# Kernel tuning notes

Measured on AMD Instinct MI355X. Metric: run time of the kernel, lower is better.

## Reference

```python
import jax, jax.numpy as jnp
import numpy as np

B, S, D = 2, 4096, 512
H, DK, DV = 8, 64, 64
LN_EPS = 1e-5
ATTN_EPS = 1e-6


def layer_norm(x, g, b):
    mu = jnp.mean(x, axis=-1, keepdims=True)
    var = jnp.var(x, axis=-1, keepdims=True)
    return (x - mu) * jax.lax.rsqrt(var + LN_EPS) * g + b


def setup_inputs() -> dict:
    key = jax.random.key(0)
    ks = jax.random.split(key, 12)
    s = 1.0 / np.sqrt(D)
    inp = {
        "Q": jax.random.normal(ks[0], (B, S, D), jnp.float32),
        "K": jax.random.normal(ks[1], (B, S, D), jnp.float32),
        "V": jax.random.normal(ks[2], (B, S, D), jnp.float32),
        "W_q": jax.random.normal(ks[3], (D, H * DK), jnp.float32) * s,
        "W_k": jax.random.normal(ks[4], (D, H * DK), jnp.float32) * s,
        "W_v": jax.random.normal(ks[5], (D, H * DV), jnp.float32) * s,
        "W_o": jax.random.normal(ks[6], (H * DV, D), jnp.float32) * s,
        "ln1_g": jnp.ones((D,), jnp.float32),
        "ln1_b": jnp.zeros((D,), jnp.float32),
        "ln2_g": jnp.ones((D,), jnp.float32),
        "ln2_b": jnp.zeros((D,), jnp.float32),
        "w1": jax.random.normal(ks[7], (4 * D, D), jnp.float32) * s,  # torch Linear: (out, in)
        "b1": jnp.zeros((4 * D,), jnp.float32),
        "w2": jax.random.normal(ks[8], (D, 4 * D), jnp.float32) * (1.0 / np.sqrt(4 * D)),
        "b2": jnp.zeros((D,), jnp.float32),
    }
    return inp


def reference(Q, K, V, W_q, W_k, W_v, W_o, ln1_g, ln1_b, ln2_g, ln2_b, w1, b1, w2, b2):
    Qn = layer_norm(Q, ln1_g, ln1_b)
    # project and split heads: [B,S,H,dk] -> [B,H,S,dk]
    q = (Qn @ W_q).reshape(B, S, H, DK).transpose(0, 2, 1, 3)
    k = (K @ W_k).reshape(B, S, H, DK).transpose(0, 2, 1, 3)
    v = (V @ W_v).reshape(B, S, H, DV).transpose(0, 2, 1, 3)
    scores = jnp.einsum("bhqd,bhkd->bhqk", q, k) / (np.sqrt(DK) + ATTN_EPS)
    attn = jax.nn.softmax(scores, axis=-1)  # same as max-subtract softmax
    ctx = jnp.einsum("bhqk,bhkd->bhqd", attn, v)
    ctx = ctx.transpose(0, 2, 1, 3).reshape(B, S, H * DV)
    att_out = ctx @ W_o  # dropout = identity (eval)
    X = Q + att_out
    Xn = layer_norm(X, ln2_g, ln2_b)
    h = jax.nn.gelu(Xn @ w1.T + b1, approximate=False)
    ffn = h @ w2.T + b2
    return X + ffn
```

## Files before the change

kernel.cpp:

```cpp
#include <hip/hip_runtime.h>

typedef unsigned short u16;
typedef __attribute__((ext_vector_type(8))) short short8;
typedef __attribute__((ext_vector_type(4))) float f32x4;

struct __align__(8) us4 { u16 x, y, z, w; };
struct __align__(8) ui2 { unsigned x, y; };

#define CEXP (1.44269504089f / (8.0f + 1e-6f))

__device__ __forceinline__ u16 f2bf(float f) {
  unsigned u = __builtin_bit_cast(unsigned, f);
  unsigned r = (u + 0x7FFFu + ((u >> 16) & 1u)) >> 16;
  return (u16)r;
}

__device__ __forceinline__ unsigned pack_bf2_trunc(float a, float b) {
  return __builtin_amdgcn_perm(__builtin_bit_cast(unsigned, b),
                               __builtin_bit_cast(unsigned, a), 0x07060302u);
}

__device__ __forceinline__ void async_load16(const void* g, void* l) {
  __builtin_amdgcn_global_load_lds((const __attribute__((address_space(1))) void*)g,
                                   (__attribute__((address_space(3))) void*)l, 16, 0, 0);
}

__global__ void prep_weights(const float* __restrict__ Wq, const float* __restrict__ Wk,
                             const float* __restrict__ Wv, const float* __restrict__ Wo,
                             const float* __restrict__ w1, const float* __restrict__ w2,
                             u16* __restrict__ wqkvT, u16* __restrict__ woT,
                             u16* __restrict__ w1b, u16* __restrict__ w2b) {
  const int z = blockIdx.y;
  const int stride = gridDim.x * blockDim.x;
  const int i0 = blockIdx.x * blockDim.x + threadIdx.x;
  if (z < 4) {
    const float* src = z == 0 ? Wq : z == 1 ? Wk : z == 2 ? Wv : Wo;
    u16* dst = z < 3 ? wqkvT + z * 512 * 512 : woT;
    const float scale = (z == 0) ? CEXP : 1.0f;
    for (int i = i0; i < 512 * 512; i += stride) {
      int n = i >> 9, k = i & 511;
      dst[i] = f2bf(src[k * 512 + n] * scale);
    }
  } else {
    const float* src = z == 4 ? w1 : w2;
    u16* dst = z == 4 ? w1b : w2b;
    for (int i = i0; i < 2048 * 512; i += stride) dst[i] = f2bf(src[i]);
  }
}

template <bool KV>
__launch_bounds__(128)
__global__ void ln_cast(const float* __restrict__ X, const float* __restrict__ gw,
                        const float* __restrict__ bw, u16* __restrict__ Y,
                        const float* __restrict__ Kin, const float* __restrict__ Vin,
                        u16* __restrict__ Kb, u16* __restrict__ Vb) {
  const int row = blockIdx.x, t = threadIdx.x;
  const size_t base = (size_t)row * 512;
  float4 x = ((const float4*)(X + base))[t];
  float s = x.x + x.y + x.z + x.w;
  float ss = x.x * x.x + x.y * x.y + x.z * x.z + x.w * x.w;
#pragma unroll
  for (int off = 32; off > 0; off >>= 1) {
    s += __shfl_xor(s, off);
    ss += __shfl_xor(ss, off);
  }
  __shared__ float red[4];
  if ((t & 63) == 0) { red[(t >> 6) * 2] = s; red[(t >> 6) * 2 + 1] = ss; }
  __syncthreads();
  const float tot = red[0] + red[2], tss = red[1] + red[3];
  const float mu = tot * (1.0f / 512.0f);
  const float var = tss * (1.0f / 512.0f) - mu * mu;
  const float rs = rsqrtf(var + 1e-5f);
  float4 g4 = ((const float4*)gw)[t];
  float4 b4 = ((const float4*)bw)[t];
  us4 o;
  o.x = f2bf((x.x - mu) * rs * g4.x + b4.x);
  o.y = f2bf((x.y - mu) * rs * g4.y + b4.y);
  o.z = f2bf((x.z - mu) * rs * g4.z + b4.z);
  o.w = f2bf((x.w - mu) * rs * g4.w + b4.w);
  ((us4*)(Y + base))[t] = o;
  if constexpr (KV) {
    float4 k4 = ((const float4*)(Kin + base))[t];
    float4 v4 = ((const float4*)(Vin + base))[t];
    us4 ko, vo;
    ko.x = f2bf(k4.x); ko.y = f2bf(k4.y); ko.z = f2bf(k4.z); ko.w = f2bf(k4.w);
    vo.x = f2bf(v4.x); vo.y = f2bf(v4.y); vo.z = f2bf(v4.z); vo.w = f2bf(v4.w);
    ((us4*)(Kb + base))[t] = ko;
    ((us4*)(Vb + base))[t] = vo;
  }
}

__launch_bounds__(256, 3)
__global__ void gemm_qkv(const u16* __restrict__ Aq, const u16* __restrict__ Ak,
                         const u16* __restrict__ Av, const u16* __restrict__ Bt,
                         u16* __restrict__ qb, u16* __restrict__ kb, u16* __restrict__ vtb) {
  __shared__ __align__(16) u16 sA[128 * 32];
  __shared__ __align__(16) u16 sB[128 * 32];
  const int tid = threadIdx.x;
  const int wave = tid >> 6, lane = tid & 63;
  const int l15 = lane & 15, quad = lane >> 4;
  const int m0 = blockIdx.x * 128, n0 = blockIdx.y * 128;
  const int sel = n0 >> 9;
  const u16* A = sel == 0 ? Aq : sel == 1 ? Ak : Av;
  const int wm = (wave >> 1) * 64, wn = (wave & 1) * 64;
  const int u0 = wave * 64 + lane, u1 = u0 + 256;
  const int K = 512;

  const u16* a0 = A + (size_t)(m0 + (u0 >> 2)) * K + (u0 & 3) * 8;
  const u16* a1 = A + (size_t)(m0 + (u1 >> 2)) * K + (u1 & 3) * 8;
  const u16* b0 = Bt + (size_t)(n0 + (u0 >> 2)) * K + (u0 & 3) * 8;
  const u16* b1p = Bt + (size_t)(n0 + (u1 >> 2)) * K + (u1 & 3) * 8;

  f32x4 acc[4][4] = {};
  for (int k0 = 0; k0 < K; k0 += 32) {
    async_load16(a0 + k0, &sA[wave * 512]);
    async_load16(a1 + k0, &sA[2048 + wave * 512]);
    async_load16(b0 + k0, &sB[wave * 512]);
    async_load16(b1p + k0, &sB[2048 + wave * 512]);
    __syncthreads();
    short8 af[4], bfr[4];
#pragma unroll
    for (int i = 0; i < 4; i++)
      af[i] = *(const short8*)&sA[(wm + i * 16 + l15) * 32 + quad * 8];
#pragma unroll
    for (int j = 0; j < 4; j++)
      bfr[j] = *(const short8*)&sB[(wn + j * 16 + l15) * 32 + quad * 8];
#pragma unroll
    for (int i = 0; i < 4; i++)
#pragma unroll
      for (int j = 0; j < 4; j++)
        acc[i][j] = __builtin_amdgcn_mfma_f32_16x16x32_bf16(af[i], bfr[j], acc[i][j], 0, 0, 0);
    __syncthreads();
  }

#pragma unroll
  for (int i = 0; i < 4; i++) {
#pragma unroll
    for (int j = 0; j < 4; j++) {
      const int ocol = ((n0 + wn) & 511) + j * 16 + l15;
      const int row0 = m0 + wm + i * 16 + quad * 4;
      if (sel < 2) {
        u16* C = sel == 0 ? qb : kb;
#pragma unroll
        for (int r = 0; r < 4; r++) C[(size_t)(row0 + r) * 512 + ocol] = f2bf(acc[i][j][r]);
      } else {
        const int b = row0 >> 12, s0 = row0 & 4095;
        const int hh = ocol >> 6, cc = ocol & 63;
        us4 pk;
        pk.x = f2bf(acc[i][j][0]); pk.y = f2bf(acc[i][j][1]);
        pk.z = f2bf(acc[i][j][2]); pk.w = f2bf(acc[i][j][3]);
        *(us4*)&vtb[((size_t)((b * 8 + hh) * 64 + cc) << 12) + s0] = pk;
      }
    }
  }
}

template <int EP, int TN, int LB>
__launch_bounds__(256, LB)
__global__ void gemm_bt(const u16* __restrict__ A, const u16* __restrict__ Bt,
                        int M, int N, int K, void* __restrict__ Cp,
                        const float* __restrict__ bias, const float* __restrict__ res) {
  constexpr int MI = (TN == 128) ? 4 : 2;
  __shared__ __align__(16) u16 sA[128 * 32];
  __shared__ __align__(16) u16 sB[TN * 32];
  const int tid = threadIdx.x;
  const int wave = tid >> 6, lane = tid & 63;
  const int l15 = lane & 15, quad = lane >> 4;
  const int m0 = blockIdx.x * 128, n0 = blockIdx.y * TN;
  const int wm = (TN == 128) ? (wave >> 1) * 64 : wave * 32;
  const int wn = (TN == 128) ? (wave & 1) * 64 : 0;
  const int u0 = wave * 64 + lane, u1 = u0 + 256;

  const u16* a0 = A + (size_t)(m0 + (u0 >> 2)) * K + (u0 & 3) * 8;
  const u16* a1 = A + (size_t)(m0 + (u1 >> 2)) * K + (u1 & 3) * 8;
  const u16* b0 = Bt + (size_t)(n0 + (u0 >> 2)) * K + (u0 & 3) * 8;

  f32x4 acc[MI][4] = {};
  for (int k0 = 0; k0 < K; k0 += 32) {
    async_load16(a0 + k0, &sA[wave * 512]);
    async_load16(a1 + k0, &sA[2048 + wave * 512]);
    async_load16(b0 + k0, &sB[wave * 512]);
    if constexpr (TN == 128) {
      const u16* b1p = Bt + (size_t)(n0 + (u1 >> 2)) * K + (u1 & 3) * 8;
      async_load16(b1p + k0, &sB[2048 + wave * 512]);
    }
    __syncthreads();
    short8 af[MI], bfr[4];
#pragma unroll
    for (int i = 0; i < MI; i++)
      af[i] = *(const short8*)&sA[(wm + i * 16 + l15) * 32 + quad * 8];
#pragma unroll
    for (int j = 0; j < 4; j++)
      bfr[j] = *(const short8*)&sB[(wn + j * 16 + l15) * 32 + quad * 8];
#pragma unroll
    for (int i = 0; i < MI; i++)
#pragma unroll
      for (int j = 0; j < 4; j++)
        acc[i][j] = __builtin_amdgcn_mfma_f32_16x16x32_bf16(af[i], bfr[j], acc[i][j], 0, 0, 0);
    __syncthreads();
  }

#pragma unroll
  for (int i = 0; i < MI; i++) {
#pragma unroll
    for (int j = 0; j < 4; j++) {
      const int col = n0 + wn + j * 16 + l15;
      const int row0 = m0 + wm + i * 16 + quad * 4;
      if (EP == 2) {
        float* C = (float*)Cp;
#pragma unroll
        for (int r = 0; r < 4; r++) {
          size_t idx = (size_t)(row0 + r) * N + col;
          C[idx] = acc[i][j][r] + res[idx];
        }
      } else if (EP == 3) {
        u16* C = (u16*)Cp;
        const float bv = bias[col];
#pragma unroll
        for (int r = 0; r < 4; r++) {
          float xx = acc[i][j][r] + bv;
          float gl = 0.5f * xx * (1.0f + erff(xx * 0.70710678118f));
          C[(size_t)(row0 + r) * N + col] = f2bf(gl);
        }
      } else {
        float* C = (float*)Cp;
        const float bv = bias[col];
#pragma unroll
        for (int r = 0; r < 4; r++) {
          size_t idx = (size_t)(row0 + r) * N + col;
          C[idx] = acc[i][j][r] + bv + res[idx];
        }
      }
    }
  }
}

__launch_bounds__(256, 3)
__global__ void attn_kernel(const u16* __restrict__ qb, const u16* __restrict__ kb,
                            const u16* __restrict__ vtb, u16* __restrict__ ctx) {
  __shared__ __align__(16) u16 sK[2 * 128 * 32];
  __shared__ __align__(16) u16 sV[4 * 64 * 32];
  __shared__ __align__(16) u16 sP[4 * 32 * 40];
  const int tid = threadIdx.x;
  const int wave = tid >> 6, lane = tid & 63;
  const int l15 = lane & 15, quad = lane >> 4;
  const int bh = blockIdx.y, b = bh >> 3, h = bh & 7;
  const int q0 = blockIdx.x * 128;
  const size_t rb = (size_t)b * 4096;

  short8 qf[2][2];
#pragma unroll
  for (int mi = 0; mi < 2; mi++)
#pragma unroll
    for (int kk = 0; kk < 2; kk++) {
      int row = q0 + wave * 32 + mi * 16 + l15;
      qf[mi][kk] = *(const short8*)&qb[(rb + row) * 512 + h * 64 + kk * 32 + quad * 8];
    }

  f32x4 o_t[2][4] = {};
  float l_part[2] = {0.f, 0.f};
  u16* myP = &sP[wave * 32 * 40];

  for (int j0 = 0; j0 < 4096; j0 += 128) {
#pragma unroll
    for (int r = 0; r < 4; r++) {
      int u = r * 256 + wave * 64 + lane;
      int kk = u >> 9, key = (u >> 2) & 127, c8 = u & 3;
      async_load16(&kb[(rb + j0 + key) * 512 + h * 64 + kk * 32 + c8 * 8],
                   &sK[(r * 256 + wave * 64) * 8]);
    }
#pragma unroll
    for (int r = 0; r < 4; r++) {
      int u = r * 256 + wave * 64 + lane;
      int kk = u >> 8, vc = (u >> 2) & 63, c8 = u & 3;
      async_load16(&vtb[((size_t)(bh * 64 + vc)) * 4096 + j0 + kk * 32 + c8 * 8],
                   &sV[(r * 256 + wave * 64) * 8]);
    }
    __syncthreads();

#pragma unroll
    for (int kk = 0; kk < 4; kk++) {
#pragma unroll
      for (int nh = 0; nh < 2; nh++) {
        const int ni = kk * 2 + nh;
        short8 af0 = *(const short8*)&sK[(ni * 16 + l15) * 32 + quad * 8];
        short8 af1 = *(const short8*)&sK[4096 + (ni * 16 + l15) * 32 + quad * 8];
#pragma unroll
        for (int mi = 0; mi < 2; mi++) {
          f32x4 st = {};
          st = __builtin_amdgcn_mfma_f32_16x16x32_bf16(af0, qf[mi][0], st, 0, 0, 0);
          st = __builtin_amdgcn_mfma_f32_16x16x32_bf16(af1, qf[mi][1], st, 0, 0, 0);
          float p0 = exp2f(st[0]), p1 = exp2f(st[1]);
          float p2 = exp2f(st[2]), p3 = exp2f(st[3]);
          l_part[mi] += (p0 + p1) + (p2 + p3);
          ui2 w;
          w.x = pack_bf2_trunc(p0, p1);
          w.y = pack_bf2_trunc(p2, p3);
          *(ui2*)&myP[(mi * 16 + l15) * 40 + nh * 16 + quad * 4] = w;
        }
      }
      asm volatile("s_waitcnt lgkmcnt(0)" ::: "memory");
      short8 pf[2], vf[4];
#pragma unroll
      for (int mi = 0; mi < 2; mi++)
        pf[mi] = *(const short8*)&myP[(mi * 16 + l15) * 40 + quad * 8];
#pragma unroll
      for (int vi = 0; vi < 4; vi++)
        vf[vi] = *(const short8*)&sV[kk * 2048 + (vi * 16 + l15) * 32 + quad * 8];
#pragma unroll
      for (int mi = 0; mi < 2; mi++)
#pragma unroll
        for (int vi = 0; vi < 4; vi++)
          o_t[mi][vi] = __builtin_amdgcn_mfma_f32_16x16x32_bf16(vf[vi], pf[mi], o_t[mi][vi], 0, 0, 0);
    }
    __syncthreads();
  }

#pragma unroll
  for (int mi = 0; mi < 2; mi++) {
    float l = l_part[mi];
    l += __shfl_xor(l, 16);
    l += __shfl_xor(l, 32);
    const float inv = 1.0f / l;
    const int row = q0 + wave * 32 + mi * 16 + l15;
#pragma unroll
    for (int vi = 0; vi < 4; vi++) {
      us4 o;
      o.x = f2bf(o_t[mi][vi][0] * inv);
      o.y = f2bf(o_t[mi][vi][1] * inv);
      o.z = f2bf(o_t[mi][vi][2] * inv);
      o.w = f2bf(o_t[mi][vi][3] * inv);
      *(us4*)&ctx[(rb + row) * 512 + h * 64 + vi * 16 + quad * 4] = o;
    }
  }
}

extern "C" void kernel_launch(void* const* d_in, const int* in_sizes, int n_in,
                              void* d_out, int out_size, void* d_ws, size_t ws_size,
                              hipStream_t stream) {
  (void)in_sizes; (void)n_in; (void)out_size; (void)ws_size;
  const float* Q = (const float*)d_in[0];
  const float* K = (const float*)d_in[1];
  const float* V = (const float*)d_in[2];
  const float* W_q = (const float*)d_in[3];
  const float* W_k = (const float*)d_in[4];
  const float* W_v = (const float*)d_in[5];
  const float* W_o = (const float*)d_in[6];
  const float* ln1_g = (const float*)d_in[7];
  const float* ln1_b = (const float*)d_in[8];
  const float* ln2_g = (const float*)d_in[9];
  const float* ln2_b = (const float*)d_in[10];
  const float* w1 = (const float*)d_in[11];
  const float* b1 = (const float*)d_in[12];
  const float* w2 = (const float*)d_in[13];
  const float* b2 = (const float*)d_in[14];

  char* w = (char*)d_ws;
  const size_t MB = 1u << 20;
  u16* wqkvT = (u16*)(w);
  u16* woT = (u16*)(w + 3 * MB / 2);
  u16* w1b = (u16*)(w + 2 * MB);
  u16* w2b = (u16*)(w + 4 * MB);
  u16* Qn  = (u16*)(w + 6 * MB);
  u16* Kb  = (u16*)(w + 14 * MB);
  u16* Vb  = (u16*)(w + 22 * MB);
  u16* qb  = (u16*)(w + 30 * MB);
  u16* kb  = (u16*)(w + 38 * MB);
  u16* vtb = (u16*)(w + 46 * MB);
  u16* ctx = (u16*)(w + 54 * MB);
  float* X = (float*)(w + 62 * MB);
  u16* Xn  = (u16*)(w + 6 * MB);
  u16* hb  = (u16*)(w + 14 * MB);

  prep_weights<<<dim3(128, 6), 256, 0, stream>>>(W_q, W_k, W_v, W_o, w1, w2,
                                                 wqkvT, woT, w1b, w2b);
  ln_cast<true><<<8192, 128, 0, stream>>>(Q, ln1_g, ln1_b, Qn, K, V, Kb, Vb);
  gemm_qkv<<<dim3(64, 12), 256, 0, stream>>>(Qn, Kb, Vb, wqkvT, qb, kb, vtb);
  attn_kernel<<<dim3(32, 16), 256, 0, stream>>>(qb, kb, vtb, ctx);
  gemm_bt<2, 64, 3><<<dim3(64, 8), 256, 0, stream>>>(ctx, woT, 8192, 512, 512, X, nullptr, Q);
  ln_cast<false><<<8192, 128, 0, stream>>>(X, ln2_g, ln2_b, Xn, nullptr, nullptr, nullptr, nullptr);
  gemm_bt<3, 128, 3><<<dim3(64, 16), 256, 0, stream>>>(Xn, w1b, 8192, 2048, 512, hb, b1, nullptr);
  gemm_bt<4, 64, 3><<<dim3(64, 8), 256, 0, stream>>>(hb, w2b, 8192, 512, 2048, (float*)d_out, b2, X);
}
```

Measured before the change: 369.9 us.

## Split attention keys across two blocks, swizzle LDS, coalesce weight prep

Attention now splits the key range in two along a new grid dimension, doubling block count, and writes unnormalized fp32 partial outputs and row sums. A new merge kernel adds the two halves, normalizes and casts to bf16. All GEMM and attention LDS tiles get an XOR swizzle of the 16-byte chunk index to cut bank conflicts. exp2f becomes the hardware intrinsic and weight-prep reads become coalesced. The cost is extra fp32 partial traffic and one more launch.

```diff
diff --git a/kernel.cpp b/kernel.cpp
--- a/kernel.cpp
+++ b/kernel.cpp
@@ -38,8 +38,8 @@
     u16* dst = z < 3 ? wqkvT + z * 512 * 512 : woT;
     const float scale = (z == 0) ? CEXP : 1.0f;
     for (int i = i0; i < 512 * 512; i += stride) {
-      int n = i >> 9, k = i & 511;
-      dst[i] = f2bf(src[k * 512 + n] * scale);
+      int k = i >> 9, n = i & 511;
+      dst[(size_t)n * 512 + k] = f2bf(src[i] * scale);
     }
   } else {
     const float* src = z == 4 ? w1 : w2;
@@ -99,17 +99,19 @@
   const int tid = threadIdx.x;
   const int wave = tid >> 6, lane = tid & 63;
   const int l15 = lane & 15, quad = lane >> 4;
+  const int qsw = (quad ^ ((l15 >> 1) & 3)) * 8;
   const int m0 = blockIdx.x * 128, n0 = blockIdx.y * 128;
   const int sel = n0 >> 9;
   const u16* A = sel == 0 ? Aq : sel == 1 ? Ak : Av;
   const int wm = (wave >> 1) * 64, wn = (wave & 1) * 64;
   const int u0 = wave * 64 + lane, u1 = u0 + 256;
+  const int sw0 = ((u0 & 3) ^ ((u0 >> 3) & 3)) * 8;
   const int K = 512;
 
-  const u16* a0 = A + (size_t)(m0 + (u0 >> 2)) * K + (u0 & 3) * 8;
-  const u16* a1 = A + (size_t)(m0 + (u1 >> 2)) * K + (u1 & 3) * 8;
-  const u16* b0 = Bt + (size_t)(n0 + (u0 >> 2)) * K + (u0 & 3) * 8;
-  const u16* b1p = Bt + (size_t)(n0 + (u1 >> 2)) * K + (u1 & 3) * 8;
+  const u16* a0 = A + (size_t)(m0 + (u0 >> 2)) * K + sw0;
+  const u16* a1 = A + (size_t)(m0 + (u1 >> 2)) * K + sw0;
+  const u16* b0 = Bt + (size_t)(n0 + (u0 >> 2)) * K + sw0;
+  const u16* b1p = Bt + (size_t)(n0 + (u1 >> 2)) * K + sw0;
 
   f32x4 acc[4][4] = {};
   for (int k0 = 0; k0 < K; k0 += 32) {
@@ -121,10 +123,10 @@
     short8 af[4], bfr[4];
 #pragma unroll
     for (int i = 0; i < 4; i++)
-      af[i] = *(const short8*)&sA[(wm + i * 16 + l15) * 32 + quad * 8];
+      af[i] = *(const short8*)&sA[(wm + i * 16 + l15) * 32 + qsw];
 #pragma unroll
     for (int j = 0; j < 4; j++)
-      bfr[j] = *(const short8*)&sB[(wn + j * 16 + l15) * 32 + quad * 8];
+      bfr[j] = *(const short8*)&sB[(wn + j * 16 + l15) * 32 + qsw];
 #pragma unroll
     for (int i = 0; i < 4; i++)
 #pragma unroll
@@ -166,14 +168,16 @@
   const int tid = threadIdx.x;
   const int wave = tid >> 6, lane = tid & 63;
   const int l15 = lane & 15, quad = lane >> 4;
+  const int qsw = (quad ^ ((l15 >> 1) & 3)) * 8;
   const int m0 = blockIdx.x * 128, n0 = blockIdx.y * TN;
   const int wm = (TN == 128) ? (wave >> 1) * 64 : wave * 32;
   const int wn = (TN == 128) ? (wave & 1) * 64 : 0;
   const int u0 = wave * 64 + lane, u1 = u0 + 256;
-
-  const u16* a0 = A + (size_t)(m0 + (u0 >> 2)) * K + (u0 & 3) * 8;
-  const u16* a1 = A + (size_t)(m0 + (u1 >> 2)) * K + (u1 & 3) * 8;
-  const u16* b0 = Bt + (size_t)(n0 + (u0 >> 2)) * K + (u0 & 3) * 8;
+  const int sw0 = ((u0 & 3) ^ ((u0 >> 3) & 3)) * 8;
+
+  const u16* a0 = A + (size_t)(m0 + (u0 >> 2)) * K + sw0;
+  const u16* a1 = A + (size_t)(m0 + (u1 >> 2)) * K + sw0;
+  const u16* b0 = Bt + (size_t)(n0 + (u0 >> 2)) * K + sw0;
 
   f32x4 acc[MI][4] = {};
   for (int k0 = 0; k0 < K; k0 += 32) {
@@ -181,17 +185,17 @@
     async_load16(a1 + k0, &sA[2048 + wave * 512]);
     async_load16(b0 + k0, &sB[wave * 512]);
     if constexpr (TN == 128) {
-      const u16* b1p = Bt + (size_t)(n0 + (u1 >> 2)) * K + (u1 & 3) * 8;
+      const u16* b1p = Bt + (size_t)(n0 + (u1 >> 2)) * K + sw0;
       async_load16(b1p + k0, &sB[2048 + wave * 512]);
     }
     __syncthreads();
     short8 af[MI], bfr[4];
 #pragma unroll
     for (int i = 0; i < MI; i++)
-      af[i] = *(const short8*)&sA[(wm + i * 16 + l15) * 32 + quad * 8];
+      af[i] = *(const short8*)&sA[(wm + i * 16 + l15) * 32 + qsw];
 #pragma unroll
     for (int j = 0; j < 4; j++)
-      bfr[j] = *(const short8*)&sB[(wn + j * 16 + l15) * 32 + quad * 8];
+      bfr[j] = *(const short8*)&sB[(wn + j * 16 + l15) * 32 + qsw];
 #pragma unroll
     for (int i = 0; i < MI; i++)
 #pragma unroll
@@ -237,15 +241,18 @@
 
 __launch_bounds__(256, 3)
 __global__ void attn_kernel(const u16* __restrict__ qb, const u16* __restrict__ kb,
-                            const u16* __restrict__ vtb, u16* __restrict__ ctx) {
+                            const u16* __restrict__ vtb, float* __restrict__ po,
+                            float* __restrict__ pl) {
   __shared__ __align__(16) u16 sK[2 * 128 * 32];
   __shared__ __align__(16) u16 sV[4 * 64 * 32];
   __shared__ __align__(16) u16 sP[4 * 32 * 40];
   const int tid = threadIdx.x;
   const int wave = tid >> 6, lane = tid & 63;
   const int l15 = lane & 15, quad = lane >> 4;
+  const int qsw = (quad ^ ((l15 >> 1) & 3)) * 8;
   const int bh = blockIdx.y, b = bh >> 3, h = bh & 7;
   const int q0 = blockIdx.x * 128;
+  const int ks = blockIdx.z;
   const size_t rb = (size_t)b * 4096;
 
   short8 qf[2][2];
@@ -261,18 +268,19 @@
   float l_part[2] = {0.f, 0.f};
   u16* myP = &sP[wave * 32 * 40];
 
-  for (int j0 = 0; j0 < 4096; j0 += 128) {
+  for (int jt = 0; jt < 16; jt++) {
+    const int j0 = ks * 2048 + jt * 128;
 #pragma unroll
     for (int r = 0; r < 4; r++) {
       int u = r * 256 + wave * 64 + lane;
-      int kk = u >> 9, key = (u >> 2) & 127, c8 = u & 3;
+      int kk = u >> 9, key = (u >> 2) & 127, c8 = (u & 3) ^ ((u >> 3) & 3);
       async_load16(&kb[(rb + j0 + key) * 512 + h * 64 + kk * 32 + c8 * 8],
                    &sK[(r * 256 + wave * 64) * 8]);
     }
 #pragma unroll
     for (int r = 0; r < 4; r++) {
       int u = r * 256 + wave * 64 + lane;
-      int kk = u >> 8, vc = (u >> 2) & 63, c8 = u & 3;
+      int kk = u >> 8, vc = (u >> 2) & 63, c8 = (u & 3) ^ ((u >> 3) & 3);
       async_load16(&vtb[((size_t)(bh * 64 + vc)) * 4096 + j0 + kk * 32 + c8 * 8],
                    &sV[(r * 256 + wave * 64) * 8]);
     }
@@ -283,20 +291,22 @@
 #pragma unroll
       for (int nh = 0; nh < 2; nh++) {
         const int ni = kk * 2 + nh;
-        short8 af0 = *(const short8*)&sK[(ni * 16 + l15) * 32 + quad * 8];
-        short8 af1 = *(const short8*)&sK[4096 + (ni * 16 + l15) * 32 + quad * 8];
+        short8 af0 = *(const short8*)&sK[(ni * 16 + l15) * 32 + qsw];
+        short8 af1 = *(const short8*)&sK[4096 + (ni * 16 + l15) * 32 + qsw];
 #pragma unroll
         for (int mi = 0; mi < 2; mi++) {
           f32x4 st = {};
           st = __builtin_amdgcn_mfma_f32_16x16x32_bf16(af0, qf[mi][0], st, 0, 0, 0);
           st = __builtin_amdgcn_mfma_f32_16x16x32_bf16(af1, qf[mi][1], st, 0, 0, 0);
-          float p0 = exp2f(st[0]), p1 = exp2f(st[1]);
-          float p2 = exp2f(st[2]), p3 = exp2f(st[3]);
+          float p0 = __builtin_amdgcn_exp2f(st[0]);
+          float p1 = __builtin_amdgcn_exp2f(st[1]);
+          float p2 = __builtin_amdgcn_exp2f(st[2]);
+          float p3 = __builtin_amdgcn_exp2f(st[3]);
           l_part[mi] += (p0 + p1) + (p2 + p3);
-          ui2 w;
-          w.x = pack_bf2_trunc(p0, p1);
-          w.y = pack_bf2_trunc(p2, p3);
-          *(ui2*)&myP[(mi * 16 + l15) * 40 + nh * 16 + quad * 4] = w;
+          ui2 wv;
+          wv.x = pack_bf2_trunc(p0, p1);
+          wv.y = pack_bf2_trunc(p2, p3);
+          *(ui2*)&myP[(mi * 16 + l15) * 40 + nh * 16 + quad * 4] = wv;
         }
       }
       asm volatile("s_waitcnt lgkmcnt(0)" ::: "memory");
@@ -306,7 +316,7 @@
         pf[mi] = *(const short8*)&myP[(mi * 16 + l15) * 40 + quad * 8];
 #pragma unroll
       for (int vi = 0; vi < 4; vi++)
-        vf[vi] = *(const short8*)&sV[kk * 2048 + (vi * 16 + l15) * 32 + quad * 8];
+        vf[vi] = *(const short8*)&sV[kk * 2048 + (vi * 16 + l15) * 32 + qsw];
 #pragma unroll
       for (int mi = 0; mi < 2; mi++)
 #pragma unroll
@@ -321,18 +331,31 @@
     float l = l_part[mi];
     l += __shfl_xor(l, 16);
     l += __shfl_xor(l, 32);
-    const float inv = 1.0f / l;
-    const int row = q0 + wave * 32 + mi * 16 + l15;
-#pragma unroll
-    for (int vi = 0; vi < 4; vi++) {
-      us4 o;
-      o.x = f2bf(o_t[mi][vi][0] * inv);
-      o.y = f2bf(o_t[mi][vi][1] * inv);
-      o.z = f2bf(o_t[mi][vi][2] * inv);
-      o.w = f2bf(o_t[mi][vi][3] * inv);
-      *(us4*)&ctx[(rb + row) * 512 + h * 64 + vi * 16 + quad * 4] = o;
-    }
-  }
+    const int qrow = q0 + wave * 32 + mi * 16 + l15;
+    if (quad == 0) pl[(size_t)ks * 65536 + (rb + qrow) * 8 + h] = l;
+#pragma unroll
+    for (int vi = 0; vi < 4; vi++)
+      *(f32x4*)&po[(size_t)ks * 4194304 + (rb + qrow) * 512 + h * 64 + vi * 16 + quad * 4] =
+          o_t[mi][vi];
+  }
+}
+
+__launch_bounds__(128)
+__global__ void attn_merge(const float* __restrict__ po, const float* __restrict__ pl,
+                           u16* __restrict__ ctx) {
+  const int row = blockIdx.x, t = threadIdx.x;
+  const int col = t * 4, h = col >> 6;
+  const size_t idx = (size_t)row * 512 + col;
+  const float l = pl[row * 8 + h] + pl[65536 + row * 8 + h];
+  f32x4 a = *(const f32x4*)&po[idx];
+  f32x4 c = *(const f32x4*)&po[4194304 + idx];
+  const float inv = 1.0f / l;
+  us4 o;
+  o.x = f2bf((a[0] + c[0]) * inv);
+  o.y = f2bf((a[1] + c[1]) * inv);
+  o.z = f2bf((a[2] + c[2]) * inv);
+  o.w = f2bf((a[3] + c[3]) * inv);
+  *(us4*)&ctx[idx] = o;
 }
 
 extern "C" void kernel_launch(void* const* d_in, const int* in_sizes, int n_in,
@@ -368,15 +391,19 @@
   u16* kb  = (u16*)(w + 38 * MB);
   u16* vtb = (u16*)(w + 46 * MB);
   u16* ctx = (u16*)(w + 54 * MB);
-  float* X = (float*)(w + 62 * MB);
-  u16* Xn  = (u16*)(w + 6 * MB);
+  float* X = (float*)(w + 94 * MB);
+  float* po = (float*)(w + 62 * MB);
+  float* pl = (float*)(w + 6 * MB);
+  u16* Xn  = (u16*)(w + 6 * MB + MB);
+  Xn = (u16*)(w + 6 * MB);
   u16* hb  = (u16*)(w + 14 * MB);
 
   prep_weights<<<dim3(128, 6), 256, 0, stream>>>(W_q, W_k, W_v, W_o, w1, w2,
                                                  wqkvT, woT, w1b, w2b);
   ln_cast<true><<<8192, 128, 0, stream>>>(Q, ln1_g, ln1_b, Qn, K, V, Kb, Vb);
   gemm_qkv<<<dim3(64, 12), 256, 0, stream>>>(Qn, Kb, Vb, wqkvT, qb, kb, vtb);
-  attn_kernel<<<dim3(32, 16), 256, 0, stream>>>(qb, kb, vtb, ctx);
+  attn_kernel<<<dim3(32, 16, 2), 256, 0, stream>>>(qb, kb, vtb, po, pl);
+  attn_merge<<<8192, 128, 0, stream>>>(po, pl, ctx);
   gemm_bt<2, 64, 3><<<dim3(64, 8), 256, 0, stream>>>(ctx, woT, 8192, 512, 512, X, nullptr, Q);
   ln_cast<false><<<8192, 128, 0, stream>>>(X, ln2_g, ln2_b, Xn, nullptr, nullptr, nullptr, nullptr);
   gemm_bt<3, 128, 3><<<dim3(64, 16), 256, 0, stream>>>(Xn, w1b, 8192, 2048, 512, hb, b1, nullptr);
```

After: 351.4 us. 1.05x faster.
